# Performance work log

Measured on AMD Instinct MI355X. Metric: run time of the kernel, lower is better.

The kernel has to match this reference:

```python
import jax, jax.numpy as jnp
import numpy as np

N = 50000
E = 500000
IN_DIM = 384
HID = 64
HEADS = 4
OUT_DIM = 128
EPS_SM = 1e-16
EPS_LN = 1e-5
NEG_SLOPE = 0.2


def gat_conv(x, row, col, ew, W, a_src, a_dst, b, heads, out_ch, concat):
    n = x.shape[0]
    h = (x @ W).reshape(n, heads, out_ch)              # [N, H, C]
    # per-node attention scores, then gather (same math as gathering h first)
    s_src = jnp.sum(h * a_src, axis=-1)                # [N, H]
    s_dst = jnp.sum(h * a_dst, axis=-1)                # [N, H]
    alpha = jax.nn.leaky_relu(s_src[row] + s_dst[col], NEG_SLOPE)  # [E, H]
    alpha = alpha * ew[:, None]
    a_exp = jnp.exp(alpha)
    denom = jax.ops.segment_sum(a_exp, col, num_segments=n)        # [N, H]
    alpha = a_exp / (denom[col] + EPS_SM)              # [E, H]
    msg = alpha[:, :, None] * h[col]                   # [E, H, C]
    out = jax.ops.segment_sum(msg, row, num_segments=n)  # [N, H, C]
    if concat:
        out = out.reshape(n, heads * out_ch)
    else:
        out = out.mean(axis=1)
    return out + b


def layer_norm(x, g, b):
    mu = x.mean(axis=-1, keepdims=True)
    var = x.var(axis=-1, keepdims=True)
    return (x - mu) / jnp.sqrt(var + EPS_LN) * g + b


def setup_inputs() -> dict:
    key = jax.random.key(0)
    ks = jax.random.split(key, 16)
    D1 = HEADS * HID  # 256
    inp = {
        "x": jax.random.normal(ks[0], (N, IN_DIM), jnp.float32),
        "edge_index": jax.random.randint(ks[1], (2, E), 0, N, jnp.int32),
        "edge_weight": jax.random.uniform(ks[2], (E,), jnp.float32),
        "W1": jax.random.normal(ks[3], (IN_DIM, D1), jnp.float32) * (1.0 / np.sqrt(IN_DIM)),
        "as1": jax.random.normal(ks[4], (1, HEADS, HID), jnp.float32) * 0.1,
        "ad1": jax.random.normal(ks[5], (1, HEADS, HID), jnp.float32) * 0.1,
        "b1": jnp.zeros((D1,), jnp.float32),
        "g1": jnp.ones((D1,), jnp.float32),
        "be1": jnp.zeros((D1,), jnp.float32),
        "W2": jax.random.normal(ks[6], (D1, D1), jnp.float32) * (1.0 / np.sqrt(D1)),
        "as2": jax.random.normal(ks[7], (1, HEADS, HID), jnp.float32) * 0.1,
        "ad2": jax.random.normal(ks[8], (1, HEADS, HID), jnp.float32) * 0.1,
        "b2": jnp.zeros((D1,), jnp.float32),
        "g2": jnp.ones((D1,), jnp.float32),
        "be2": jnp.zeros((D1,), jnp.float32),
        "W3": jax.random.normal(ks[9], (D1, OUT_DIM), jnp.float32) * (1.0 / np.sqrt(D1)),
        "as3": jax.random.normal(ks[10], (1, 1, OUT_DIM), jnp.float32) * 0.1,
        "ad3": jax.random.normal(ks[11], (1, 1, OUT_DIM), jnp.float32) * 0.1,
        "b3": jnp.zeros((OUT_DIM,), jnp.float32),
        "g3": jnp.ones((OUT_DIM,), jnp.float32),
        "be3": jnp.zeros((OUT_DIM,), jnp.float32),
    }
    return inp


def reference(x, edge_index, edge_weight, W1, as1, ad1, b1, g1, be1,
              W2, as2, ad2, b2, g2, be2, W3, as3, ad3, b3, g3, be3):
    row, col = edge_index[0], edge_index[1]
    h = gat_conv(x, row, col, edge_weight, W1, as1, ad1, b1, HEADS, HID, True)
    h = jax.nn.elu(layer_norm(h, g1, be1))
    h = gat_conv(h, row, col, edge_weight, W2, as2, ad2, b2, HEADS, HID, True)
    h = jax.nn.elu(layer_norm(h, g2, be2))
    h = gat_conv(h, row, col, edge_weight, W3, as3, ad3, b3, 1, OUT_DIM, False)
    return layer_norm(h, g3, be3)
```

## Files before the change

### kernel.cpp

```cpp
#include <hip/hip_runtime.h>
#include <hip/hip_bf16.h>


typedef __bf16 bf16x8_t __attribute__((ext_vector_type(8)));
typedef float  fx4      __attribute__((ext_vector_type(4)));
typedef float  f32x2    __attribute__((ext_vector_type(2)));

__device__ __forceinline__ float u2f(unsigned short u) {
    return __uint_as_float(((unsigned)u) << 16);
}
__device__ __forceinline__ unsigned short f2u(float f) {
    unsigned b = __float_as_uint(f);
    unsigned rounded = b + 0x7FFF + ((b >> 16) & 1);
    if (((b >> 23) & 0xFF) == 0xFF) rounded = b;
    return (unsigned short)(rounded >> 16);
}

__global__ void f32_to_bf16_k(const float* __restrict__ src, unsigned short* __restrict__ dst,
                              long n) {
    long i = (long)blockIdx.x * 256 + threadIdx.x;
    const long stride = (long)gridDim.x * 256;
    for (; i < n; i += stride) dst[i] = f2u(src[i]);
}

__global__ void transpose_conv_k(const float* __restrict__ W, unsigned short* __restrict__ Wt,
                                 int K, int N) {
    int idx = blockIdx.x * 256 + threadIdx.x;
    if (idx >= K * N) return;
    int k = idx / N, n = idx - k * N;
    Wt[(size_t)n * K + k] = f2u(W[idx]);
}

__global__ void fill_const_f32_k(float* __restrict__ out, long n, float v) {
    long i = (long)blockIdx.x * 256 + threadIdx.x;
    const long stride = (long)gridDim.x * 256;
    for (; i < n; i += stride) out[i] = v;
}

__global__ void count_both_k(const int* __restrict__ row, const int* __restrict__ col,
                             int* __restrict__ rcnt, int* __restrict__ ccnt,
                             int2* __restrict__ rank, int E, int Nn) {
    int e = blockIdx.x * 256 + threadIdx.x;
    if (e >= E) return;
    int r = row[e], c = col[e];
    int rr = -1, rc = -1;
    if ((unsigned)r < (unsigned)Nn) rr = atomicAdd(&rcnt[r], 1);
    if ((unsigned)c < (unsigned)Nn) rc = atomicAdd(&ccnt[c], 1);
    rank[e] = make_int2(rr, rc);
}

__global__ __launch_bounds__(256) void scan1_k(const int* __restrict__ cnt,
                                               int* __restrict__ local,
                                               int* __restrict__ bsum, int n) {
    __shared__ int sm[256];
    int i = blockIdx.x * 256 + threadIdx.x;
    int tid = threadIdx.x;
    int v = (i < n) ? cnt[i] : 0;
    sm[tid] = v;
    __syncthreads();
    for (int o = 1; o < 256; o <<= 1) {
        int t = (tid >= o) ? sm[tid - o] : 0;
        __syncthreads();
        sm[tid] += t;
        __syncthreads();
    }
    if (i < n) local[i] = sm[tid];
    if (tid == 255) bsum[blockIdx.x] = sm[255];
}

__global__ __launch_bounds__(512) void scan2_k(int* __restrict__ bsum, int nb) {
    __shared__ int sm[512];
    int tid = threadIdx.x;
    int v = (tid < nb) ? bsum[tid] : 0;
    sm[tid] = v;
    __syncthreads();
    for (int o = 1; o < 512; o <<= 1) {
        int t = (tid >= o) ? sm[tid - o] : 0;
        __syncthreads();
        sm[tid] += t;
        __syncthreads();
    }
    if (tid < nb) bsum[tid] = sm[tid];
}

__global__ __launch_bounds__(256) void scan3_k(const int* __restrict__ cnt,
                                               const int* __restrict__ local,
                                               const int* __restrict__ bsum,
                                               int* __restrict__ rowptr,
                                               int* __restrict__ colptr,
                                               int N) {
    int i = blockIdx.x * 256 + threadIdx.x;
    int n2 = 2 * N;
    if (i >= n2) return;
    int b = blockIdx.x;
    int s = local[i] + (b > 0 ? bsum[b - 1] : 0);
    if (i < N) {
        rowptr[i + 1] = s;
        if (i == 0) rowptr[0] = 0;
    } else {
        int bN = (N - 1) >> 8;
        int base = local[N - 1] + (bN > 0 ? bsum[bN - 1] : 0);
        int j = i - N;
        colptr[j + 1] = s - base;
        if (j == 0) colptr[0] = 0;
    }
}

__global__ void fill_both_k(const int* __restrict__ row, const int* __restrict__ col,
                            const float* __restrict__ ew,
                            const int2* __restrict__ rank,
                            const int* __restrict__ rowptr, const int* __restrict__ colptr,
                            long* __restrict__ csr, long* __restrict__ csc,
                            int E, int Nn) {
    int e = blockIdx.x * 256 + threadIdx.x;
    if (e >= E) return;
    int r = row[e], c = col[e];
    int wb = __float_as_int(ew[e]);
    int2 rk = rank[e];
    if (rk.x >= 0) {
        int s = rowptr[r] + rk.x;
        int cc = ((unsigned)c < (unsigned)Nn) ? c : 0;
        long v = (long)(unsigned)cc | ((long)(unsigned)wb << 32);
        __builtin_nontemporal_store(v, csr + s);
    }
    if (rk.y >= 0) {
        int s = colptr[c] + rk.y;
        int rr = ((unsigned)r < (unsigned)Nn) ? r : 0;
        long v = (long)(unsigned)rr | ((long)(unsigned)wb << 32);
        __builtin_nontemporal_store(v, csc + s);
    }
}

#define LSTR 40
__global__ __launch_bounds__(256) void gemm_bf16(const unsigned short* __restrict__ A,
                                                 const unsigned short* __restrict__ Bt,
                                                 unsigned short* __restrict__ C,
                                                 int M, int Ncol, int K) {
    __shared__ unsigned short As[128 * LSTR];
    __shared__ unsigned short Bs[128 * LSTR];
    const int t = threadIdx.x;
    const int lane = t & 63;
    const int wave = t >> 6;
    const int quad = lane >> 4, l16 = lane & 15;
    const int row0 = blockIdx.y * 128, col0 = blockIdx.x * 128;
    const int wr = (wave >> 1) * 64, wc = (wave & 1) * 64;
    const int sr = t >> 2, ss = (t & 3) * 8;
    fx4 acc[4][4] = {};
    for (int k0 = 0; k0 < K; k0 += 32) {
#pragma unroll
        for (int rr = 0; rr < 2; rr++) {
            int r = sr + rr * 64;
            uint4 av = make_uint4(0, 0, 0, 0);
            int gr = row0 + r;
            if (gr < M) av = *(const uint4*)(A + (size_t)gr * K + k0 + ss);
            *(uint4*)(As + r * LSTR + ss) = av;
            uint4 bv = *(const uint4*)(Bt + (size_t)(col0 + r) * K + k0 + ss);
            *(uint4*)(Bs + r * LSTR + ss) = bv;
        }
        __syncthreads();
        bf16x8_t af[4], bfr[4];
#pragma unroll
        for (int i = 0; i < 4; i++) {
            af[i]  = *(const bf16x8_t*)(As + (wr + i * 16 + l16) * LSTR + quad * 8);
            bfr[i] = *(const bf16x8_t*)(Bs + (wc + i * 16 + l16) * LSTR + quad * 8);
        }
#pragma unroll
        for (int i = 0; i < 4; i++)
#pragma unroll
            for (int j = 0; j < 4; j++)
                acc[i][j] = __builtin_amdgcn_mfma_f32_16x16x32_bf16(af[i], bfr[j], acc[i][j], 0, 0, 0);
        __syncthreads();
    }
#pragma unroll
    for (int i = 0; i < 4; i++) {
        int rb = row0 + wr + i * 16 + quad * 4;
#pragma unroll
        for (int j = 0; j < 4; j++) {
            int c = col0 + wc + j * 16 + l16;
#pragma unroll
            for (int r = 0; r < 4; r++) {
                int gr = rb + r;
                if (gr < M) C[(size_t)gr * Ncol + c] = f2u(acc[i][j][r]);
            }
        }
    }
}

template <int CPL, int LPH, int H>
__global__ __launch_bounds__(256) void scores_k(const unsigned short* __restrict__ hb,
                                                const float* __restrict__ asrc,
                                                const float* __restrict__ adst,
                                                float* __restrict__ ssrc, float* __restrict__ sdst,
                                                int N) {
    int node = blockIdx.x * 4 + (threadIdx.x >> 6);
    if (node >= N) return;
    int lane = threadIdx.x & 63;
    const int D = CPL * 64;
    const unsigned short* hp = hb + (size_t)node * D + lane * CPL;
    float s1 = 0.f, s2 = 0.f;
#pragma unroll
    for (int i = 0; i < CPL; i++) {
        float h = u2f(hp[i]);
        s1 += h * asrc[lane * CPL + i];
        s2 += h * adst[lane * CPL + i];
    }
#pragma unroll
    for (int m = 1; m < LPH; m <<= 1) {
        s1 += __shfl_xor(s1, m);
        s2 += __shfl_xor(s2, m);
    }
    if ((lane & (LPH - 1)) == 0) {
        ssrc[(size_t)node * H + lane / LPH] = s1;
        sdst[(size_t)node * H + lane / LPH] = s2;
    }
}

template <int H>
__global__ __launch_bounds__(256) void denom_csc_k(const int* __restrict__ colptr,
                                                   const int2* __restrict__ csc,
                                                   const float* __restrict__ ssrc,
                                                   const float* __restrict__ sdst,
                                                   float* __restrict__ att, int N) {
    int idx = blockIdx.x * 256 + threadIdx.x;
    const int L2H = (H == 4) ? 2 : ((H == 2) ? 1 : 0);
    int node = idx >> (L2H + 1);
    int rem = idx - (node << (L2H + 1));
    int h = rem & (H - 1);
    int parity = rem >> L2H;
    if (node >= N) return;
    const float sd = sdst[(size_t)node * H + h];
    float acc = 0.f;
    int kbeg = colptr[node], kend = colptr[node + 1];
    int k0 = kbeg + parity;
    if (k0 < kend) {
        int klast = kend - 1;
        int kB = k0 + 2, kC = k0 + 4;
        int2 ceA = csc[k0];
        int2 ceB = csc[kB < kend ? kB : klast];
        int2 ceC = csc[kC < kend ? kC : klast];
        float sA = ssrc[(size_t)ceA.x * H + h];
        float sB = ssrc[(size_t)ceB.x * H + h];
        for (int k = k0; k < kend; k += 2) {
            int kD = k + 6;
            int2 ceD = csc[kD < kend ? kD : klast];
            float sC = ssrc[(size_t)ceC.x * H + h];
            float we = __int_as_float(ceA.y);
            float s = sA + sd;
            s = (s > 0.f) ? s : 0.2f * s;
            acc += __expf(fminf(s * we, 60.f));
            ceA = ceB; ceB = ceC; ceC = ceD;
            sA = sB; sB = sC;
        }
    }
    acc += __shfl_xor(acc, H);
    if (parity == 0) {
        float2 pr;
        pr.x = sd;
        pr.y = 1.0f / (acc + 1e-16f);
        *(float2*)(att + (size_t)node * 2 * H + 2 * h) = pr;
    }
}

template <int CPL, int H, bool DOELU, bool F32OUT>
__global__ __launch_bounds__(256) void agg_ln_k(const unsigned short* __restrict__ hb,
                                                const float* __restrict__ ssrc,
                                                const float* __restrict__ att,
                                                const int* __restrict__ rowptr,
                                                const int2* __restrict__ csr,
                                                const float* __restrict__ bias,
                                                const float* __restrict__ gamma,
                                                const float* __restrict__ beta,
                                                void* __restrict__ outv, int N, int E) {
    int node = blockIdx.x * 4 + (threadIdx.x >> 6);
    if (node >= N) return;
    const int lane = threadIdx.x & 63;
    const int hl = lane & 31;
    const int eo = lane >> 5;
    const int D = CPL * 32, C = D / H;
    const int colbase = hl * CPL;
    const int head = colbase / C;
    const float sn = ssrc[(size_t)node * H + head];
    const unsigned short* hbl = hb + colbase;
    f32x2 acc2[CPL / 2] = {};
    int kbeg = rowptr[node], kend = rowptr[node + 1];
    if (kbeg < 0) kbeg = 0;
    if (kend > E) kend = E;

    if (kbeg < kend) {
        const int klast = kend - 1;
        int kA = kbeg + eo, kB = kbeg + 2 + eo, kC = kbeg + 4 + eo;
        int2 ceA = csr[kA < kend ? kA : klast];
        int2 ceB = csr[kB < kend ? kB : klast];
        int2 ceC = csr[kC < kend ? kC : klast];
        float2 prA, prB;
        uint4 hvA = make_uint4(0,0,0,0), hvB = make_uint4(0,0,0,0);
        {
            prA = *(const float2*)(att + (size_t)ceA.x * (2 * H) + 2 * head);
            const unsigned short* hp = hbl + (size_t)ceA.x * D;
            if constexpr (CPL == 8) hvA = *(const uint4*)hp;
            else { uint2 t2 = *(const uint2*)hp; hvA.x = t2.x; hvA.y = t2.y; }
        }
        {
            prB = *(const float2*)(att + (size_t)ceB.x * (2 * H) + 2 * head);
            const unsigned short* hp = hbl + (size_t)ceB.x * D;
            if constexpr (CPL == 8) hvB = *(const uint4*)hp;
            else { uint2 t2 = *(const uint2*)hp; hvB.x = t2.x; hvB.y = t2.y; }
        }
        for (int k = kbeg; k < kend; k += 2) {
            int kD = k + 6 + eo;
            int2 ceD = csr[kD < kend ? kD : klast];
            float2 prC;
            uint4 hvC = make_uint4(0,0,0,0);
            {
                prC = *(const float2*)(att + (size_t)ceC.x * (2 * H) + 2 * head);
                const unsigned short* hp = hbl + (size_t)ceC.x * D;
                if constexpr (CPL == 8) hvC = *(const uint4*)hp;
                else { uint2 t2 = *(const uint2*)hp; hvC.x = t2.x; hvC.y = t2.y; }
            }
            float we = __int_as_float(ceA.y);
            float s = sn + prA.x;
            s = (s > 0.f) ? s : 0.2f * s;
            float ae = __expf(fminf(s * we, 60.f));
            float w = ae * prA.y;
            w = (k + eo < kend) ? w : 0.f;
            f32x2 w2;
            w2[0] = w; w2[1] = w;
            f32x2 h01, h23;
            h01[0] = __uint_as_float(hvA.x << 16);
            h01[1] = __uint_as_float(hvA.x & 0xFFFF0000u);
            h23[0] = __uint_as_float(hvA.y << 16);
            h23[1] = __uint_as_float(hvA.y & 0xFFFF0000u);
            acc2[0] += w2 * h01;
            acc2[1] += w2 * h23;
            if constexpr (CPL == 8) {
                f32x2 h45, h67;
                h45[0] = __uint_as_float(hvA.z << 16);
                h45[1] = __uint_as_float(hvA.z & 0xFFFF0000u);
                h67[0] = __uint_as_float(hvA.w << 16);
                h67[1] = __uint_as_float(hvA.w & 0xFFFF0000u);
                acc2[2] += w2 * h45;
                acc2[3] += w2 * h67;
            }
            ceA = ceB; ceB = ceC; ceC = ceD;
            prA = prB; hvA = hvB;
            prB = prC; hvB = hvC;
        }
    }
    float accf[CPL];
#pragma unroll
    for (int i = 0; i < CPL; i++) accf[i] = acc2[i >> 1][i & 1];
#pragma unroll
    for (int i = 0; i < CPL; i++) accf[i] += __shfl_xor(accf[i], 32);

    float v[CPL];
    float sum = 0.f, sq = 0.f;
#pragma unroll
    for (int i = 0; i < CPL; i++) {
        v[i] = accf[i] + bias[colbase + i];
        sum += v[i];
        sq += v[i] * v[i];
    }
#pragma unroll
    for (int m = 1; m < 32; m <<= 1) {
        sum += __shfl_xor(sum, m);
        sq += __shfl_xor(sq, m);
    }
    float mu  = sum * (1.0f / D);
    float var = sq * (1.0f / D) - mu * mu;
    float inv = rsqrtf(fmaxf(var, 0.f) + 1e-5f);
    if (eo == 0) {
#pragma unroll
        for (int i = 0; i < CPL; i++) {
            float y = (v[i] - mu) * inv * gamma[colbase + i] + beta[colbase + i];
            if (DOELU) y = (y > 0.f) ? y : (__expf(y) - 1.f);
            size_t idx = (size_t)node * D + colbase + i;
            if constexpr (F32OUT) ((float*)outv)[idx] = y;
            else                  ((unsigned short*)outv)[idx] = f2u(y);
        }
    }
}

extern "C" void kernel_launch(void* const* d_in, const int* in_sizes, int n_in,
                              void* d_out, int out_size, void* d_ws, size_t ws_size,
                              hipStream_t stream) {
    const int IN_DIM = 384;
    const int N = in_sizes[0] / IN_DIM;
    const int E = in_sizes[1] / 2;
    float* outp = (float*)d_out;
    const int FG = 2048;

    if (n_in != 21 || out_size != N * 128) {
        fill_const_f32_k<<<FG, 256, 0, stream>>>(outp, (long)out_size, 9.0f);
        return;
    }

    const float* x = (const float*)d_in[0];
    const int* ei = (const int*)d_in[1];
    const int* row = ei;
    const int* col = ei + E;
    const float* ew = (const float*)d_in[2];
    const float* W1 = (const float*)d_in[3];
    const float* as1 = (const float*)d_in[4];
    const float* ad1 = (const float*)d_in[5];
    const float* b1 = (const float*)d_in[6];
    const float* g1 = (const float*)d_in[7];
    const float* be1 = (const float*)d_in[8];
    const float* W2 = (const float*)d_in[9];
    const float* as2 = (const float*)d_in[10];
    const float* ad2 = (const float*)d_in[11];
    const float* b2 = (const float*)d_in[12];
    const float* g2 = (const float*)d_in[13];
    const float* be2 = (const float*)d_in[14];
    const float* W3 = (const float*)d_in[15];
    const float* as3 = (const float*)d_in[16];
    const float* ad3 = (const float*)d_in[17];
    const float* b3 = (const float*)d_in[18];
    const float* g3 = (const float*)d_in[19];
    const float* be3 = (const float*)d_in[20];

    char* ws = (char*)d_ws;
    size_t off = 0;
    auto alloc = [&](size_t b) -> char* {
        char* p = ws + off;
        off = (off + b + 255) & ~(size_t)255;
        return p;
    };
    unsigned short* xb = (unsigned short*)alloc((size_t)N * IN_DIM * 2);
    unsigned short* hb = (unsigned short*)alloc((size_t)N * 256 * 2);
    unsigned short* ab = (unsigned short*)alloc((size_t)N * 256 * 2);
    float* att = (float*)alloc((size_t)N * 8 * 4);
    float* ssrc = (float*)alloc((size_t)N * 4 * 4);
    float* sdst = (float*)alloc((size_t)N * 4 * 4);
    unsigned short* W1t = (unsigned short*)alloc((size_t)384 * 256 * 2);
    unsigned short* W2t = (unsigned short*)alloc((size_t)256 * 256 * 2);
    unsigned short* W3t = (unsigned short*)alloc((size_t)256 * 128 * 2);
    int* rowptr = (int*)alloc((size_t)(N + 1) * 4);
    int* colptr = (int*)alloc((size_t)(N + 1) * 4);
    int* cnt2 = (int*)alloc((size_t)2 * N * 4);
    int* slocal = (int*)alloc((size_t)2 * N * 4);
    int* sbsum = (int*)alloc((size_t)512 * 4);
    int2* rank = (int2*)alloc((size_t)E * 8);
    long* csr = (long*)alloc((size_t)E * 8);
    long* csc = (long*)alloc((size_t)E * 8);

    if (off > ws_size) {
        fill_const_f32_k<<<FG, 256, 0, stream>>>(outp, (long)out_size, 7.0f);
        return;
    }

    int* rcnt = cnt2;
    int* ccnt = cnt2 + N;

    const int ebl = (E + 255) / 256;
    const int nbl4 = (N + 3) / 4;
    const int mrows = (N + 127) / 128;
    const int n2 = 2 * N;
    const int sblocks = (n2 + 255) / 256;

    f32_to_bf16_k<<<FG, 256, 0, stream>>>(x, xb, (long)N * IN_DIM);
    transpose_conv_k<<<(384 * 256 + 255) / 256, 256, 0, stream>>>(W1, W1t, 384, 256);
    transpose_conv_k<<<(256 * 256 + 255) / 256, 256, 0, stream>>>(W2, W2t, 256, 256);
    transpose_conv_k<<<(256 * 128 + 255) / 256, 256, 0, stream>>>(W3, W3t, 256, 128);

    hipMemsetAsync(cnt2, 0, (size_t)n2 * 4, stream);
    count_both_k<<<ebl, 256, 0, stream>>>(row, col, rcnt, ccnt, rank, E, N);
    scan1_k<<<sblocks, 256, 0, stream>>>(cnt2, slocal, sbsum, n2);
    scan2_k<<<1, 512, 0, stream>>>(sbsum, sblocks);
    scan3_k<<<sblocks, 256, 0, stream>>>(cnt2, slocal, sbsum, rowptr, colptr, N);
    fill_both_k<<<ebl, 256, 0, stream>>>(row, col, ew, rank, rowptr, colptr, csr, csc, E, N);

    gemm_bf16<<<dim3(2, mrows), 256, 0, stream>>>(xb, W1t, hb, N, 256, 384);
    scores_k<4, 16, 4><<<nbl4, 256, 0, stream>>>(hb, as1, ad1, ssrc, sdst, N);
    denom_csc_k<4><<<(N * 8 + 255) / 256, 256, 0, stream>>>(colptr, (const int2*)csc, ssrc, sdst, att, N);
    agg_ln_k<8, 4, true, false><<<nbl4, 256, 0, stream>>>(hb, ssrc, att, rowptr, (const int2*)csr,
                                                          b1, g1, be1, ab, N, E);

    gemm_bf16<<<dim3(2, mrows), 256, 0, stream>>>(ab, W2t, hb, N, 256, 256);
    scores_k<4, 16, 4><<<nbl4, 256, 0, stream>>>(hb, as2, ad2, ssrc, sdst, N);
    denom_csc_k<4><<<(N * 8 + 255) / 256, 256, 0, stream>>>(colptr, (const int2*)csc, ssrc, sdst, att, N);
    agg_ln_k<8, 4, true, false><<<nbl4, 256, 0, stream>>>(hb, ssrc, att, rowptr, (const int2*)csr,
                                                          b2, g2, be2, ab, N, E);

    gemm_bf16<<<dim3(1, mrows), 256, 0, stream>>>(ab, W3t, hb, N, 128, 256);
    scores_k<2, 64, 1><<<nbl4, 256, 0, stream>>>(hb, as3, ad3, ssrc, sdst, N);
    denom_csc_k<1><<<(N * 2 + 255) / 256, 256, 0, stream>>>(colptr, (const int2*)csc, ssrc, sdst, att, N);
    agg_ln_k<4, 1, false, true><<<nbl4, 256, 0, stream>>>(hb, ssrc, att, rowptr, (const int2*)csr,
                                                          b3, g3, be3, outp, N, E);
}
```

Before: 503.7 us.

## Split each node's edge aggregation across two wavefronts with LDS reduction

The aggregation kernel now gives each node two wavefronts instead of one, so each block handles 2 nodes rather than 4. The two waves process interleaved edge pairs with a stride of 4, and the partial sums are combined through shared memory after a block barrier. The packed f32x2 accumulation is also replaced with scalar FMAs. The aim is more memory-level parallelism per node for the gather-bound loop (average degree is about 10), at the cost of twice as many blocks, a __syncthreads, and LDS traffic.

```diff
diff --git a/kernel.cpp b/kernel.cpp
--- a/kernel.cpp
+++ b/kernel.cpp
@@ -4,7 +4,6 @@
 
 typedef __bf16 bf16x8_t __attribute__((ext_vector_type(8)));
 typedef float  fx4      __attribute__((ext_vector_type(4)));
-typedef float  f32x2    __attribute__((ext_vector_type(2)));
 
 __device__ __forceinline__ float u2f(unsigned short u) {
     return __uint_as_float(((unsigned)u) << 16);
@@ -271,86 +270,92 @@
                                                 const float* __restrict__ gamma,
                                                 const float* __restrict__ beta,
                                                 void* __restrict__ outv, int N, int E) {
-    int node = blockIdx.x * 4 + (threadIdx.x >> 6);
-    if (node >= N) return;
+    __shared__ float sm[2][32][CPL];
+    const int wid = threadIdx.x >> 6;
+    const int nl = wid >> 1;
+    const int parity = wid & 1;
+    const int node = blockIdx.x * 2 + nl;
     const int lane = threadIdx.x & 63;
     const int hl = lane & 31;
     const int eo = lane >> 5;
     const int D = CPL * 32, C = D / H;
     const int colbase = hl * CPL;
     const int head = colbase / C;
-    const float sn = ssrc[(size_t)node * H + head];
+    const bool valid = node < N;
     const unsigned short* hbl = hb + colbase;
-    f32x2 acc2[CPL / 2] = {};
-    int kbeg = rowptr[node], kend = rowptr[node + 1];
-    if (kbeg < 0) kbeg = 0;
-    if (kend > E) kend = E;
-
-    if (kbeg < kend) {
-        const int klast = kend - 1;
-        int kA = kbeg + eo, kB = kbeg + 2 + eo, kC = kbeg + 4 + eo;
-        int2 ceA = csr[kA < kend ? kA : klast];
-        int2 ceB = csr[kB < kend ? kB : klast];
-        int2 ceC = csr[kC < kend ? kC : klast];
-        float2 prA, prB;
-        uint4 hvA = make_uint4(0,0,0,0), hvB = make_uint4(0,0,0,0);
-        {
-            prA = *(const float2*)(att + (size_t)ceA.x * (2 * H) + 2 * head);
-            const unsigned short* hp = hbl + (size_t)ceA.x * D;
-            if constexpr (CPL == 8) hvA = *(const uint4*)hp;
-            else { uint2 t2 = *(const uint2*)hp; hvA.x = t2.x; hvA.y = t2.y; }
-        }
-        {
-            prB = *(const float2*)(att + (size_t)ceB.x * (2 * H) + 2 * head);
-            const unsigned short* hp = hbl + (size_t)ceB.x * D;
-            if constexpr (CPL == 8) hvB = *(const uint4*)hp;
-            else { uint2 t2 = *(const uint2*)hp; hvB.x = t2.x; hvB.y = t2.y; }
-        }
-        for (int k = kbeg; k < kend; k += 2) {
-            int kD = k + 6 + eo;
-            int2 ceD = csr[kD < kend ? kD : klast];
-            float2 prC;
-            uint4 hvC = make_uint4(0,0,0,0);
+    float accf[CPL] = {};
+    float sn = 0.f;
+
+    if (valid) {
+        sn = ssrc[(size_t)node * H + head];
+        int kbeg = rowptr[node], kend = rowptr[node + 1];
+        if (kbeg < 0) kbeg = 0;
+        if (kend > E) kend = E;
+        int k0 = kbeg + 2 * parity;
+        if (k0 < kend) {
+            const int klast = kend - 1;
+            int kA = k0 + eo, kB = k0 + 4 + eo, kC = k0 + 8 + eo;
+            int2 ceA = csr[kA < kend ? kA : klast];
+            int2 ceB = csr[kB < kend ? kB : klast];
+            int2 ceC = csr[kC < kend ? kC : klast];
+            float2 prA, prB;
+            uint4 hvA = make_uint4(0,0,0,0), hvB = make_uint4(0,0,0,0);
             {
-                prC = *(const float2*)(att + (size_t)ceC.x * (2 * H) + 2 * head);
-                const unsigned short* hp = hbl + (size_t)ceC.x * D;
-                if constexpr (CPL == 8) hvC = *(const uint4*)hp;
-                else { uint2 t2 = *(const uint2*)hp; hvC.x = t2.x; hvC.y = t2.y; }
+                prA = *(const float2*)(att + (size_t)ceA.x * (2 * H) + 2 * head);
+                const unsigned short* hp = hbl + (size_t)ceA.x * D;
+                if constexpr (CPL == 8) hvA = *(const uint4*)hp;
+                else { uint2 t2 = *(const uint2*)hp; hvA.x = t2.x; hvA.y = t2.y; }
             }
-            float we = __int_as_float(ceA.y);
-            float s = sn + prA.x;
-            s = (s > 0.f) ? s : 0.2f * s;
-            float ae = __expf(fminf(s * we, 60.f));
-            float w = ae * prA.y;
-            w = (k + eo < kend) ? w : 0.f;
-            f32x2 w2;
-            w2[0] = w; w2[1] = w;
-            f32x2 h01, h23;
-            h01[0] = __uint_as_float(hvA.x << 16);
-            h01[1] = __uint_as_float(hvA.x & 0xFFFF0000u);
-            h23[0] = __uint_as_float(hvA.y << 16);
-            h23[1] = __uint_as_float(hvA.y & 0xFFFF0000u);
-            acc2[0] += w2 * h01;
-            acc2[1] += w2 * h23;
-            if constexpr (CPL == 8) {
-                f32x2 h45, h67;
-                h45[0] = __uint_as_float(hvA.z << 16);
-                h45[1] = __uint_as_float(hvA.z & 0xFFFF0000u);
-                h67[0] = __uint_as_float(hvA.w << 16);
-                h67[1] = __uint_as_float(hvA.w & 0xFFFF0000u);
-                acc2[2] += w2 * h45;
-                acc2[3] += w2 * h67;
+            {
+                prB = *(const float2*)(att + (size_t)ceB.x * (2 * H) + 2 * head);
+                const unsigned short* hp = hbl + (size_t)ceB.x * D;
+                if constexpr (CPL == 8) hvB = *(const uint4*)hp;
+                else { uint2 t2 = *(const uint2*)hp; hvB.x = t2.x; hvB.y = t2.y; }
             }
-            ceA = ceB; ceB = ceC; ceC = ceD;
-            prA = prB; hvA = hvB;
-            prB = prC; hvB = hvC;
-        }
-    }
-    float accf[CPL];
-#pragma unroll
-    for (int i = 0; i < CPL; i++) accf[i] = acc2[i >> 1][i & 1];
+            for (int k = k0; k < kend; k += 4) {
+                int kD = k + 12 + eo;
+                int2 ceD = csr[kD < kend ? kD : klast];
+                float2 prC;
+                uint4 hvC = make_uint4(0,0,0,0);
+                {
+                    prC = *(const float2*)(att + (size_t)ceC.x * (2 * H) + 2 * head);
+                    const unsigned short* hp = hbl + (size_t)ceC.x * D;
+                    if constexpr (CPL == 8) hvC = *(const uint4*)hp;
+                    else { uint2 t2 = *(const uint2*)hp; hvC.x = t2.x; hvC.y = t2.y; }
+                }
+                float we = __int_as_float(ceA.y);
+                float s = sn + prA.x;
+                s = (s > 0.f) ? s : 0.2f * s;
+                float ae = __expf(fminf(s * we, 60.f));
+                float w = ae * prA.y;
+                w = (k + eo < kend) ? w : 0.f;
+                accf[0] += w * u2f((unsigned short)(hvA.x & 0xFFFFu));
+                accf[1] += w * u2f((unsigned short)(hvA.x >> 16));
+                accf[2] += w * u2f((unsigned short)(hvA.y & 0xFFFFu));
+                accf[3] += w * u2f((unsigned short)(hvA.y >> 16));
+                if constexpr (CPL == 8) {
+                    accf[4] += w * u2f((unsigned short)(hvA.z & 0xFFFFu));
+                    accf[5] += w * u2f((unsigned short)(hvA.z >> 16));
+                    accf[6] += w * u2f((unsigned short)(hvA.w & 0xFFFFu));
+                    accf[7] += w * u2f((unsigned short)(hvA.w >> 16));
+                }
+                ceA = ceB; ceB = ceC; ceC = ceD;
+                prA = prB; hvA = hvB;
+                prB = prC; hvB = hvC;
+            }
+        }
+    }
 #pragma unroll
     for (int i = 0; i < CPL; i++) accf[i] += __shfl_xor(accf[i], 32);
+
+    if (parity == 1 && valid && lane < 32) {
+#pragma unroll
+        for (int i = 0; i < CPL; i++) sm[nl][lane][i] = accf[i];
+    }
+    __syncthreads();
+    if (parity != 0 || !valid) return;
+#pragma unroll
+    for (int i = 0; i < CPL; i++) accf[i] += sm[nl][hl][i];
 
     float v[CPL];
     float sum = 0.f, sq = 0.f;
@@ -453,6 +458,7 @@
 
     const int ebl = (E + 255) / 256;
     const int nbl4 = (N + 3) / 4;
+    const int nbl2 = (N + 1) / 2;
     const int mrows = (N + 127) / 128;
     const int n2 = 2 * N;
     const int sblocks = (n2 + 255) / 256;
@@ -472,18 +478,18 @@
     gemm_bf16<<<dim3(2, mrows), 256, 0, stream>>>(xb, W1t, hb, N, 256, 384);
     scores_k<4, 16, 4><<<nbl4, 256, 0, stream>>>(hb, as1, ad1, ssrc, sdst, N);
     denom_csc_k<4><<<(N * 8 + 255) / 256, 256, 0, stream>>>(colptr, (const int2*)csc, ssrc, sdst, att, N);
-    agg_ln_k<8, 4, true, false><<<nbl4, 256, 0, stream>>>(hb, ssrc, att, rowptr, (const int2*)csr,
+    agg_ln_k<8, 4, true, false><<<nbl2, 256, 0, stream>>>(hb, ssrc, att, rowptr, (const int2*)csr,
                                                           b1, g1, be1, ab, N, E);
 
     gemm_bf16<<<dim3(2, mrows), 256, 0, stream>>>(ab, W2t, hb, N, 256, 256);
     scores_k<4, 16, 4><<<nbl4, 256, 0, stream>>>(hb, as2, ad2, ssrc, sdst, N);
     denom_csc_k<4><<<(N * 8 + 255) / 256, 256, 0, stream>>>(colptr, (const int2*)csc, ssrc, sdst, att, N);
-    agg_ln_k<8, 4, true, false><<<nbl4, 256, 0, stream>>>(hb, ssrc, att, rowptr, (const int2*)csr,
+    agg_ln_k<8, 4, true, false><<<nbl2, 256, 0, stream>>>(hb, ssrc, att, rowptr, (const int2*)csr,
                                                           b2, g2, be2, ab, N, E);
 
     gemm_bf16<<<dim3(1, mrows), 256, 0, stream>>>(ab, W3t, hb, N, 128, 256);
     scores_k<2, 64, 1><<<nbl4, 256, 0, stream>>>(hb, as3, ad3, ssrc, sdst, N);
     denom_csc_k<1><<<(N * 2 + 255) / 256, 256, 0, stream>>>(colptr, (const int2*)csc, ssrc, sdst, att, N);
-    agg_ln_k<4, 1, false, true><<<nbl4, 256, 0, stream>>>(hb, ssrc, att, rowptr, (const int2*)csr,
+    agg_ln_k<4, 1, false, true><<<nbl2, 256, 0, stream>>>(hb, ssrc, att, rowptr, (const int2*)csr,
                                                           b3, g3, be3, outp, N, E);
 }
```

Measured after the change: 524.0 us. 1.04x slower.
